# Performance work log

Hardware: AMD Instinct MI355X
Metric: run time of the kernel (lower is better)

## Reference

```python
import jax, jax.numpy as jnp
import numpy as np

H = 32          # hidden_size
IN = 32         # input_size
OUT = 1         # output_size
B, T = 4096, 168


def setup_inputs() -> dict:
    key = jax.random.key(0)
    ks = jax.random.split(key, 8)
    k = 1.0 / np.sqrt(H)  # torch nn.RNN init bound
    u = lambda kk, shape: jax.random.uniform(kk, shape, jnp.float32, -k, k)
    return {
        "x": jax.random.normal(ks[0], (B, T, IN), jnp.float32),
        "hidden": jax.random.normal(ks[1], (1, B, H), jnp.float32),
        "W_ih": u(ks[2], (H, IN)),
        "W_hh": u(ks[3], (H, H)),
        "b_ih": u(ks[4], (H,)),
        "b_hh": u(ks[5], (H,)),
        "W_out": u(ks[6], (OUT, H)),
        "b_out": u(ks[7], (OUT,)),
    }


def reference(x, hidden, W_ih, W_hh, b_ih, b_hh, W_out, b_out):
    # Elman RNN, relu nonlinearity, single layer, batch_first.
    # h_t = relu(x_t @ W_ih^T + b_ih + h_{t-1} @ W_hh^T + b_hh)
    h0 = hidden[0]                                   # [B, H]
    # Precompute the input projection for all timesteps in one big GEMM.
    xp = jnp.einsum('bti,hi->bth', x, W_ih) + (b_ih + b_hh)  # [B, T, H]
    xp_t = jnp.swapaxes(xp, 0, 1)                    # [T, B, H]

    def step(h, xt):
        h = jax.nn.relu(xt + h @ W_hh.T)
        return h, None

    hT, _ = jax.lax.scan(step, h0, xp_t)             # hT: [B, H] (last step)
    pred = hT @ W_out.T + b_out                      # [B, OUT]
    return pred, hT[None]                            # hidden: [1, B, H]
```

## Files before the change

### kernel.cpp

```cpp
#include <hip/hip_runtime.h>

#define HD 32
#define DP 12

typedef __attribute__((ext_vector_type(8))) short bf16x8;
typedef __attribute__((ext_vector_type(4))) float f32x4;

__device__ __forceinline__ int cvtpk_bf16(float a, float b) {
    int r;
    asm("v_cvt_pk_bf16_f32 %0, %1, %2" : "=v"(r) : "v"(a), "v"(b));
    return r;
}

__device__ __forceinline__ void split_pair(float a, float b, int& hi, int& lo) {
    hi = cvtpk_bf16(a, b);
    float fa = __int_as_float(hi << 16);
    float fb = __int_as_float((unsigned)hi & 0xffff0000u);
    lo = cvtpk_bf16(a - fa, b - fb);
}

__device__ __forceinline__ bf16x8 pack4(int w0, int w1, int w2, int w3) {
    union { int i[4]; bf16x8 v; } u;
    u.i[0] = w0; u.i[1] = w1; u.i[2] = w2; u.i[3] = w3;
    return u.v;
}

__device__ __forceinline__ void split_frag(f32x4 a, f32x4 b, bf16x8& hi, bf16x8& lo) {
    int h0,h1,h2,h3,l0,l1,l2,l3;
    split_pair(a[0], a[1], h0, l0);
    split_pair(a[2], a[3], h1, l1);
    split_pair(b[0], b[1], h2, l2);
    split_pair(b[2], b[3], h3, l3);
    hi = pack4(h0,h1,h2,h3);
    lo = pack4(l0,l1,l2,l3);
}

__device__ __forceinline__ bf16x8 to_bf16_frag(f32x4 a, f32x4 b) {
    return pack4(cvtpk_bf16(a[0], a[1]), cvtpk_bf16(a[2], a[3]),
                 cvtpk_bf16(b[0], b[1]), cvtpk_bf16(b[2], b[3]));
}

__device__ __forceinline__ int pk_relu(int v) {
    int r;
    asm("v_pk_max_f16 %0, %1, 0" : "=v"(r) : "v"(v));
    return r;
}

__device__ __forceinline__ void gload_pair(f32x4& a, f32x4& b, const float* sbase, int voff) {
    asm volatile("global_load_dwordx4 %0, %2, %3\n\t"
                 "global_load_dwordx4 %1, %2, %3 offset:16"
                 : "=&v"(a), "=&v"(b) : "v"(voff), "s"(sbase));
}

#define WAIT_TIE2(N, a, b) \
    asm volatile("s_waitcnt vmcnt(" #N ")" : "+v"(a), "+v"(b))
#define WAIT_TIE4(N, a, b, c, d) \
    asm volatile("s_waitcnt vmcnt(" #N ")" : "+v"(a), "+v"(b), "+v"(c), "+v"(d))

#define MFMA(a,b,c) __builtin_amdgcn_mfma_f32_16x16x32_bf16((a),(b),(c),0,0,0)

__global__ __launch_bounds__(64, 1)
void rnn_v7(const float* __restrict__ x,
            const float* __restrict__ h0p,
            const float* __restrict__ W_ih,
            const float* __restrict__ W_hh,
            const float* __restrict__ b_ih,
            const float* __restrict__ b_hh,
            const float* __restrict__ W_out,
            const float* __restrict__ b_out,
            float* __restrict__ out,
            int B, int T)
{
    const int l = threadIdx.x;
    const int q = l >> 4;
    const int c = l & 15;
    const int bglob = blockIdx.x * 16 + c;

    const int rA0 = ((c >> 2) << 3) + (c & 3);
    const int rA1 = rA0 + 4;

    bf16x8 Whh0h, Whh0l, Whh1h, Whh1l, Wih0, Wih1;
    {
        const f32x4* p;
        p = (const f32x4*)(W_hh + rA0 * HD + q * 8); split_frag(p[0], p[1], Whh0h, Whh0l);
        p = (const f32x4*)(W_hh + rA1 * HD + q * 8); split_frag(p[0], p[1], Whh1h, Whh1l);
        p = (const f32x4*)(W_ih + rA0 * HD + q * 8); Wih0 = to_bf16_frag(p[0], p[1]);
        p = (const f32x4*)(W_ih + rA1 * HD + q * 8); Wih1 = to_bf16_frag(p[0], p[1]);
    }

    f32x4 bias0, bias1;
#pragma unroll
    for (int r = 0; r < 4; ++r) {
        bias0[r] = b_ih[q*8 + r]     + b_hh[q*8 + r];
        bias1[r] = b_ih[q*8 + 4 + r] + b_hh[q*8 + 4 + r];
    }

    bf16x8 h_bf;
    {
        const f32x4* p = (const f32x4*)(h0p + (size_t)bglob * HD + q * 8);
        h_bf = to_bf16_frag(p[0], p[1]);
    }

    const int voff = (int)(((size_t)bglob * T * HD + q * 8) * 4);

    f32x4 xa[DP], xb[DP];
#pragma unroll
    for (int s = 0; s < DP; ++s)
        gload_pair(xa[s], xb[s], x + (size_t)s * HD, voff);

    f32x4 xpA0, xpA1, xpB0, xpB1;
    {
        WAIT_TIE2(22, xa[0], xb[0]);
        bf16x8 xbf = to_bf16_frag(xa[0], xb[0]);
        xpA0 = MFMA(Wih0, xbf, bias0);
        xpA1 = MFMA(Wih1, xbf, bias1);
    }
    {
        WAIT_TIE2(20, xa[1], xb[1]);
        bf16x8 xbf = to_bf16_frag(xa[1], xb[1]);
        xpB0 = MFMA(Wih0, xbf, bias0);
        xpB1 = MFMA(Wih1, xbf, bias1);
    }

    f32x4 hA = {0,0,0,0}, hB = {0,0,0,0};

    for (int t0 = 0; t0 < T; t0 += DP) {
#pragma unroll
        for (int s = 0; s < DP; s += 2) {
            const int t = t0 + s;
            f32x4 a0 = MFMA(Whh0h, h_bf, xpA0);
            f32x4 a1 = MFMA(Whh1h, h_bf, xpA1);
            a0 = MFMA(Whh0l, h_bf, a0);
            a1 = MFMA(Whh1l, h_bf, a1);

            int k1 = t + DP;     k1 = (k1 < T) ? k1 : (T - 1);
            int k2 = t + DP + 1; k2 = (k2 < T) ? k2 : (T - 1);
            gload_pair(xa[s],     xb[s],     x + (size_t)k1 * HD, voff);
            gload_pair(xa[s + 1], xb[s + 1], x + (size_t)k2 * HD, voff);

            const int s2 = (s + 2) % DP;
            const int s3 = (s + 3) % DP;
            WAIT_TIE4(20, xa[s2], xb[s2], xa[s3], xb[s3]);

            {
                bf16x8 xbf = to_bf16_frag(xa[s2], xb[s2]);
                xpA0 = MFMA(Wih0, xbf, bias0);
                xpA1 = MFMA(Wih1, xbf, bias1);
            }

            h_bf = pack4(pk_relu(cvtpk_bf16(a0[0], a0[1])),
                         pk_relu(cvtpk_bf16(a0[2], a0[3])),
                         pk_relu(cvtpk_bf16(a1[0], a1[1])),
                         pk_relu(cvtpk_bf16(a1[2], a1[3])));

            f32x4 b0 = MFMA(Whh0h, h_bf, xpB0);
            f32x4 b1 = MFMA(Whh1h, h_bf, xpB1);
            b0 = MFMA(Whh0l, h_bf, b0);
            b1 = MFMA(Whh1l, h_bf, b1);

            {
                bf16x8 xbf = to_bf16_frag(xa[s3], xb[s3]);
                xpB0 = MFMA(Wih0, xbf, bias0);
                xpB1 = MFMA(Wih1, xbf, bias1);
            }

            h_bf = pack4(pk_relu(cvtpk_bf16(b0[0], b0[1])),
                         pk_relu(cvtpk_bf16(b0[2], b0[3])),
                         pk_relu(cvtpk_bf16(b1[0], b1[1])),
                         pk_relu(cvtpk_bf16(b1[2], b1[3])));
            hA = b0; hB = b1;
        }
    }

#pragma unroll
    for (int r = 0; r < 4; ++r) {
        hA[r] = fmaxf(hA[r], 0.0f);
        hB[r] = fmaxf(hB[r], 0.0f);
    }

    float* outh = out + B + (size_t)bglob * HD;
#pragma unroll
    for (int r = 0; r < 4; ++r) {
        outh[q*8 + r]     = hA[r];
        outh[q*8 + 4 + r] = hB[r];
    }
    float p = 0.0f;
#pragma unroll
    for (int r = 0; r < 4; ++r)
        p += hA[r] * W_out[q*8 + r] + hB[r] * W_out[q*8 + 4 + r];
    p += __shfl_xor(p, 16, 64);
    p += __shfl_xor(p, 32, 64);
    if (q == 0) out[bglob] = p + b_out[0];
}

extern "C" void kernel_launch(void* const* d_in, const int* in_sizes, int n_in,
                              void* d_out, int out_size, void* d_ws, size_t ws_size,
                              hipStream_t stream) {
    const float* x      = (const float*)d_in[0];
    const float* hidden = (const float*)d_in[1];
    const float* W_ih   = (const float*)d_in[2];
    const float* W_hh   = (const float*)d_in[3];
    const float* b_ih   = (const float*)d_in[4];
    const float* b_hh   = (const float*)d_in[5];
    const float* W_out  = (const float*)d_in[6];
    const float* b_out  = (const float*)d_in[7];
    float* out = (float*)d_out;

    const int B = in_sizes[1] / HD;
    const int T = in_sizes[0] / (B * HD);

    rnn_v7<<<dim3(B / 16), dim3(64), 0, stream>>>(
        x, hidden, W_ih, W_hh, b_ih, b_hh, W_out, b_out, out, B, T);
}
```

Measured before the change: 23.42 us.

## Split into producer wave for input projection and consumer wave for recurrence via LDS

Each block now runs two waves: wave 1 streams x from global memory, computes the input projection with MFMA, and writes it into a 16-slot LDS ring buffer. Wave 0 runs only the recurrent MFMA chain, reading the precomputed projections from LDS with lookahead. Taking global loads and projection MFMAs off the serial recurrence path is meant to shorten the critical path per timestep. In exchange it adds LDS traffic and a block barrier every four steps, and relies on T being a multiple of 8.

```diff
diff --git a/kernel.cpp b/kernel.cpp
--- a/kernel.cpp
+++ b/kernel.cpp
@@ -1,7 +1,6 @@
 #include <hip/hip_runtime.h>
 
 #define HD 32
-#define DP 12
 
 typedef __attribute__((ext_vector_type(8))) short bf16x8;
 typedef __attribute__((ext_vector_type(4))) float f32x4;
@@ -46,21 +45,32 @@
     return r;
 }
 
-__device__ __forceinline__ void gload_pair(f32x4& a, f32x4& b, const float* sbase, int voff) {
-    asm volatile("global_load_dwordx4 %0, %2, %3\n\t"
-                 "global_load_dwordx4 %1, %2, %3 offset:16"
-                 : "=&v"(a), "=&v"(b) : "v"(voff), "s"(sbase));
-}
-
-#define WAIT_TIE2(N, a, b) \
-    asm volatile("s_waitcnt vmcnt(" #N ")" : "+v"(a), "+v"(b))
-#define WAIT_TIE4(N, a, b, c, d) \
-    asm volatile("s_waitcnt vmcnt(" #N ")" : "+v"(a), "+v"(b), "+v"(c), "+v"(d))
+__device__ __forceinline__ void gload_quad(f32x4& a1, f32x4& b1, f32x4& a2, f32x4& b2,
+                                           const float* sbase, int voff) {
+    asm volatile("global_load_dwordx4 %0, %4, %5\n\t"
+                 "global_load_dwordx4 %1, %4, %5 offset:16\n\t"
+                 "global_load_dwordx4 %2, %4, %5 offset:128\n\t"
+                 "global_load_dwordx4 %3, %4, %5 offset:144"
+                 : "=&v"(a1), "=&v"(b1), "=&v"(a2), "=&v"(b2)
+                 : "v"(voff), "s"(sbase));
+}
+
+#define WAIT_VM8(N,a0,b0,a1,b1,a2,b2,a3,b3) \
+    asm volatile("s_waitcnt vmcnt(" #N ")" : "+v"(a0),"+v"(b0),"+v"(a1),"+v"(b1), \
+                                             "+v"(a2),"+v"(b2),"+v"(a3),"+v"(b3))
+#define WAIT_LGKM2(N, a, b) \
+    asm volatile("s_waitcnt lgkmcnt(" #N ")" : "+v"(a), "+v"(b))
+
+__device__ __forceinline__ void lds_read_pair(f32x4& a, f32x4& b, unsigned addr) {
+    asm volatile("ds_read_b128 %0, %2\n\t"
+                 "ds_read_b128 %1, %2 offset:16384"
+                 : "=&v"(a), "=&v"(b) : "v"(addr));
+}
 
 #define MFMA(a,b,c) __builtin_amdgcn_mfma_f32_16x16x32_bf16((a),(b),(c),0,0,0)
 
-__global__ __launch_bounds__(64, 1)
-void rnn_v7(const float* __restrict__ x,
+__global__ __launch_bounds__(128, 1)
+void rnn_pc(const float* __restrict__ x,
             const float* __restrict__ h0p,
             const float* __restrict__ W_ih,
             const float* __restrict__ W_hh,
@@ -71,126 +81,159 @@
             float* __restrict__ out,
             int B, int T)
 {
-    const int l = threadIdx.x;
-    const int q = l >> 4;
-    const int c = l & 15;
+    __shared__ __align__(16) f32x4 smX[2][16][64];
+
+    const int tid = threadIdx.x;
+    const int wid = tid >> 6;
+    const int l   = tid & 63;
+    const int q   = l >> 4;
+    const int c   = l & 15;
     const int bglob = blockIdx.x * 16 + c;
-
     const int rA0 = ((c >> 2) << 3) + (c & 3);
     const int rA1 = rA0 + 4;
-
-    bf16x8 Whh0h, Whh0l, Whh1h, Whh1l, Wih0, Wih1;
-    {
-        const f32x4* p;
-        p = (const f32x4*)(W_hh + rA0 * HD + q * 8); split_frag(p[0], p[1], Whh0h, Whh0l);
-        p = (const f32x4*)(W_hh + rA1 * HD + q * 8); split_frag(p[0], p[1], Whh1h, Whh1l);
-        p = (const f32x4*)(W_ih + rA0 * HD + q * 8); Wih0 = to_bf16_frag(p[0], p[1]);
-        p = (const f32x4*)(W_ih + rA1 * HD + q * 8); Wih1 = to_bf16_frag(p[0], p[1]);
+    const int NPH2 = T / 8;
+
+    if (wid == 1) {
+        bf16x8 Wih0, Wih1;
+        {
+            const f32x4* p;
+            p = (const f32x4*)(W_ih + rA0*HD + q*8); Wih0 = to_bf16_frag(p[0], p[1]);
+            p = (const f32x4*)(W_ih + rA1*HD + q*8); Wih1 = to_bf16_frag(p[0], p[1]);
+        }
+        f32x4 bias0, bias1;
+#pragma unroll
+        for (int r = 0; r < 4; ++r) {
+            bias0[r] = b_ih[q*8 + r]     + b_hh[q*8 + r];
+            bias1[r] = b_ih[q*8 + 4 + r] + b_hh[q*8 + 4 + r];
+        }
+        const int voff = (int)(((size_t)bglob * T * HD + q * 8) * 4);
+
+        f32x4 xa[8], xb[8];
+        gload_quad(xa[0],xb[0],xa[1],xb[1], x + (size_t)0*HD, voff);
+        gload_quad(xa[2],xb[2],xa[3],xb[3], x + (size_t)2*HD, voff);
+        gload_quad(xa[4],xb[4],xa[5],xb[5], x + (size_t)4*HD, voff);
+        gload_quad(xa[6],xb[6],xa[7],xb[7], x + (size_t)6*HD, voff);
+        WAIT_VM8(8, xa[0],xb[0],xa[1],xb[1],xa[2],xb[2],xa[3],xb[3]);
+#pragma unroll
+        for (int i = 0; i < 4; ++i) {
+            bf16x8 xbf = to_bf16_frag(xa[i], xb[i]);
+            smX[0][i][l] = MFMA(Wih0, xbf, bias0);
+            smX[1][i][l] = MFMA(Wih1, xbf, bias1);
+        }
+        WAIT_VM8(0, xa[4],xb[4],xa[5],xb[5],xa[6],xb[6],xa[7],xb[7]);
+#pragma unroll
+        for (int i = 4; i < 8; ++i) {
+            bf16x8 xbf = to_bf16_frag(xa[i], xb[i]);
+            smX[0][i][l] = MFMA(Wih0, xbf, bias0);
+            smX[1][i][l] = MFMA(Wih1, xbf, bias1);
+        }
+        gload_quad(xa[0],xb[0],xa[1],xb[1], x + (size_t) 8*HD, voff);
+        gload_quad(xa[2],xb[2],xa[3],xb[3], x + (size_t)10*HD, voff);
+        gload_quad(xa[4],xb[4],xa[5],xb[5], x + (size_t)12*HD, voff);
+        gload_quad(xa[6],xb[6],xa[7],xb[7], x + (size_t)14*HD, voff);
+        asm volatile("s_waitcnt lgkmcnt(0)" ::: "memory");
+        __builtin_amdgcn_s_barrier();
+
+        for (int p2 = 0; p2 < NPH2; ++p2) {
+            const int tE = 8*p2 + 8;
+            WAIT_VM8(8, xa[0],xb[0],xa[1],xb[1],xa[2],xb[2],xa[3],xb[3]);
+#pragma unroll
+            for (int i = 0; i < 4; ++i) {
+                bf16x8 xbf = to_bf16_frag(xa[i], xb[i]);
+                const int sl = (tE + i) & 15;
+                smX[0][sl][l] = MFMA(Wih0, xbf, bias0);
+                smX[1][sl][l] = MFMA(Wih1, xbf, bias1);
+            }
+            {
+                int t1 = tE + 8;  if (t1 > T-2) t1 = T-2;
+                int t2 = tE + 10; if (t2 > T-2) t2 = T-2;
+                gload_quad(xa[0],xb[0],xa[1],xb[1], x + (size_t)t1*HD, voff);
+                gload_quad(xa[2],xb[2],xa[3],xb[3], x + (size_t)t2*HD, voff);
+            }
+            asm volatile("s_waitcnt lgkmcnt(0)" ::: "memory");
+            __builtin_amdgcn_s_barrier();
+            const int tO = 8*p2 + 12;
+            WAIT_VM8(8, xa[4],xb[4],xa[5],xb[5],xa[6],xb[6],xa[7],xb[7]);
+#pragma unroll
+            for (int i = 0; i < 4; ++i) {
+                bf16x8 xbf = to_bf16_frag(xa[4+i], xb[4+i]);
+                const int sl = (tO + i) & 15;
+                smX[0][sl][l] = MFMA(Wih0, xbf, bias0);
+                smX[1][sl][l] = MFMA(Wih1, xbf, bias1);
+            }
+            {
+                int t1 = tO + 8;  if (t1 > T-2) t1 = T-2;
+                int t2 = tO + 10; if (t2 > T-2) t2 = T-2;
+                gload_quad(xa[4],xb[4],xa[5],xb[5], x + (size_t)t1*HD, voff);
+                gload_quad(xa[6],xb[6],xa[7],xb[7], x + (size_t)t2*HD, voff);
+            }
+            asm volatile("s_waitcnt lgkmcnt(0)" ::: "memory");
+            __builtin_amdgcn_s_barrier();
+        }
+    } else {
+        bf16x8 Whh0h, Whh0l, Whh1h, Whh1l;
+        {
+            const f32x4* p;
+            p = (const f32x4*)(W_hh + rA0*HD + q*8); split_frag(p[0], p[1], Whh0h, Whh0l);
+            p = (const f32x4*)(W_hh + rA1*HD + q*8); split_frag(p[0], p[1], Whh1h, Whh1l);
+        }
+        bf16x8 h_bf;
+        {
+            const f32x4* p = (const f32x4*)(h0p + (size_t)bglob * HD + q * 8);
+            h_bf = to_bf16_frag(p[0], p[1]);
+        }
+        const unsigned lbase = (unsigned)(uintptr_t)&smX[0][0][l];
+
+        f32x4 rdA[4], rdB[4];
+        f32x4 hA = {0,0,0,0}, hB = {0,0,0,0};
+
+        __builtin_amdgcn_s_barrier();
+        asm volatile("" ::: "memory");
+        lds_read_pair(rdA[0], rdB[0], lbase);
+        lds_read_pair(rdA[1], rdB[1], lbase + 1024);
+
+        const int NPH = 2 * NPH2;
+        for (int k = 0; k < NPH; ++k) {
+            const int t0 = 4 * k;
+#pragma unroll
+            for (int i = 0; i < 4; ++i) {
+                WAIT_LGKM2(2, rdA[i], rdB[i]);
+                f32x4 a0 = MFMA(Whh0h, h_bf, rdA[i]);
+                f32x4 a1 = MFMA(Whh1h, h_bf, rdB[i]);
+                a0 = MFMA(Whh0l, h_bf, a0);
+                a1 = MFMA(Whh1l, h_bf, a1);
+                lds_read_pair(rdA[(i+2)&3], rdB[(i+2)&3],
+                              lbase + (unsigned)(((t0 + i + 2) & 15) * 1024));
+                h_bf = pack4(pk_relu(cvtpk_bf16(a0[0], a0[1])),
+                             pk_relu(cvtpk_bf16(a0[2], a0[3])),
+                             pk_relu(cvtpk_bf16(a1[0], a1[1])),
+                             pk_relu(cvtpk_bf16(a1[2], a1[3])));
+                hA = a0; hB = a1;
+            }
+            asm volatile("" ::: "memory");
+            __builtin_amdgcn_s_barrier();
+            asm volatile("" ::: "memory");
+        }
+
+#pragma unroll
+        for (int r = 0; r < 4; ++r) {
+            hA[r] = fmaxf(hA[r], 0.0f);
+            hB[r] = fmaxf(hB[r], 0.0f);
+        }
+        float* outh = out + B + (size_t)bglob * HD;
+#pragma unroll
+        for (int r = 0; r < 4; ++r) {
+            outh[q*8 + r]     = hA[r];
+            outh[q*8 + 4 + r] = hB[r];
+        }
+        float p = 0.0f;
+#pragma unroll
+        for (int r = 0; r < 4; ++r)
+            p += hA[r] * W_out[q*8 + r] + hB[r] * W_out[q*8 + 4 + r];
+        p += __shfl_xor(p, 16, 64);
+        p += __shfl_xor(p, 32, 64);
+        if (q == 0) out[bglob] = p + b_out[0];
     }
-
-    f32x4 bias0, bias1;
-#pragma unroll
-    for (int r = 0; r < 4; ++r) {
-        bias0[r] = b_ih[q*8 + r]     + b_hh[q*8 + r];
-        bias1[r] = b_ih[q*8 + 4 + r] + b_hh[q*8 + 4 + r];
-    }
-
-    bf16x8 h_bf;
-    {
-        const f32x4* p = (const f32x4*)(h0p + (size_t)bglob * HD + q * 8);
-        h_bf = to_bf16_frag(p[0], p[1]);
-    }
-
-    const int voff = (int)(((size_t)bglob * T * HD + q * 8) * 4);
-
-    f32x4 xa[DP], xb[DP];
-#pragma unroll
-    for (int s = 0; s < DP; ++s)
-        gload_pair(xa[s], xb[s], x + (size_t)s * HD, voff);
-
-    f32x4 xpA0, xpA1, xpB0, xpB1;
-    {
-        WAIT_TIE2(22, xa[0], xb[0]);
-        bf16x8 xbf = to_bf16_frag(xa[0], xb[0]);
-        xpA0 = MFMA(Wih0, xbf, bias0);
-        xpA1 = MFMA(Wih1, xbf, bias1);
-    }
-    {
-        WAIT_TIE2(20, xa[1], xb[1]);
-        bf16x8 xbf = to_bf16_frag(xa[1], xb[1]);
-        xpB0 = MFMA(Wih0, xbf, bias0);
-        xpB1 = MFMA(Wih1, xbf, bias1);
-    }
-
-    f32x4 hA = {0,0,0,0}, hB = {0,0,0,0};
-
-    for (int t0 = 0; t0 < T; t0 += DP) {
-#pragma unroll
-        for (int s = 0; s < DP; s += 2) {
-            const int t = t0 + s;
-            f32x4 a0 = MFMA(Whh0h, h_bf, xpA0);
-            f32x4 a1 = MFMA(Whh1h, h_bf, xpA1);
-            a0 = MFMA(Whh0l, h_bf, a0);
-            a1 = MFMA(Whh1l, h_bf, a1);
-
-            int k1 = t + DP;     k1 = (k1 < T) ? k1 : (T - 1);
-            int k2 = t + DP + 1; k2 = (k2 < T) ? k2 : (T - 1);
-            gload_pair(xa[s],     xb[s],     x + (size_t)k1 * HD, voff);
-            gload_pair(xa[s + 1], xb[s + 1], x + (size_t)k2 * HD, voff);
-
-            const int s2 = (s + 2) % DP;
-            const int s3 = (s + 3) % DP;
-            WAIT_TIE4(20, xa[s2], xb[s2], xa[s3], xb[s3]);
-
-            {
-                bf16x8 xbf = to_bf16_frag(xa[s2], xb[s2]);
-                xpA0 = MFMA(Wih0, xbf, bias0);
-                xpA1 = MFMA(Wih1, xbf, bias1);
-            }
-
-            h_bf = pack4(pk_relu(cvtpk_bf16(a0[0], a0[1])),
-                         pk_relu(cvtpk_bf16(a0[2], a0[3])),
-                         pk_relu(cvtpk_bf16(a1[0], a1[1])),
-                         pk_relu(cvtpk_bf16(a1[2], a1[3])));
-
-            f32x4 b0 = MFMA(Whh0h, h_bf, xpB0);
-            f32x4 b1 = MFMA(Whh1h, h_bf, xpB1);
-            b0 = MFMA(Whh0l, h_bf, b0);
-            b1 = MFMA(Whh1l, h_bf, b1);
-
-            {
-                bf16x8 xbf = to_bf16_frag(xa[s3], xb[s3]);
-                xpB0 = MFMA(Wih0, xbf, bias0);
-                xpB1 = MFMA(Wih1, xbf, bias1);
-            }
-
-            h_bf = pack4(pk_relu(cvtpk_bf16(b0[0], b0[1])),
-                         pk_relu(cvtpk_bf16(b0[2], b0[3])),
-                         pk_relu(cvtpk_bf16(b1[0], b1[1])),
-                         pk_relu(cvtpk_bf16(b1[2], b1[3])));
-            hA = b0; hB = b1;
-        }
-    }
-
-#pragma unroll
-    for (int r = 0; r < 4; ++r) {
-        hA[r] = fmaxf(hA[r], 0.0f);
-        hB[r] = fmaxf(hB[r], 0.0f);
-    }
-
-    float* outh = out + B + (size_t)bglob * HD;
-#pragma unroll
-    for (int r = 0; r < 4; ++r) {
-        outh[q*8 + r]     = hA[r];
-        outh[q*8 + 4 + r] = hB[r];
-    }
-    float p = 0.0f;
-#pragma unroll
-    for (int r = 0; r < 4; ++r)
-        p += hA[r] * W_out[q*8 + r] + hB[r] * W_out[q*8 + 4 + r];
-    p += __shfl_xor(p, 16, 64);
-    p += __shfl_xor(p, 32, 64);
-    if (q == 0) out[bglob] = p + b_out[0];
 }
 
 extern "C" void kernel_launch(void* const* d_in, const int* in_sizes, int n_in,
@@ -209,6 +252,6 @@
     const int B = in_sizes[1] / HD;
     const int T = in_sizes[0] / (B * HD);
 
-    rnn_v7<<<dim3(B / 16), dim3(64), 0, stream>>>(
+    rnn_pc<<<dim3(B / 16), dim3(128), 0, stream>>>(
         x, hidden, W_ih, W_hh, b_ih, b_hh, W_out, b_out, out, B, T);
 }
```

New measurement: 23.69 us. About the same (+1.2%).
